# Kernel optimization log

Hardware: AMD Instinct MI355X
Metric: run time of the kernel (lower is better)

## Reference

```python
import jax, jax.numpy as jnp
import numpy as np

N = 300000
MAX_TORSION = 7
MAX_RIGID = 8
MAX_SS = 3
MAX_ATOM = 24
NRES = 22
EPS = 1e-6


def v_norm_safe(v):
    # normalize last dim with epsilon clamp (torch v_norm_safe analogue)
    return v / jnp.clip(jnp.linalg.norm(v, axis=-1, keepdims=True), EPS)


def combine_operations(X, Y):
    # X, Y: [..., 4, 3] rigid ops (3x3 rotation rows + 1 translation row)
    rot = X[..., :3, :] @ Y[..., :3, :]
    t = jnp.einsum('...ij,...j->...i', X[..., :3, :], Y[..., 3, :]) + X[..., 3, :]
    return jnp.concatenate([rot, t[..., None, :]], axis=-2)


def setup_inputs() -> dict:
    key = jax.random.key(0)
    ks = jax.random.split(key, 9)
    return {
        'output_0': jax.random.normal(ks[0], (N, 2 * MAX_TORSION + MAX_SS, 1), jnp.float32),
        'output_1': jax.random.normal(ks[1], (N, 3, 3), jnp.float32),
        'pos': jax.random.normal(ks[2], (N, 3), jnp.float32),
        'ss': jax.random.randint(ks[3], (N,), 0, MAX_SS),
        'residue_type': jax.random.randint(ks[4], (N,), 0, NRES),
        'rigid_transforms': jax.random.normal(ks[5], (MAX_SS, NRES, MAX_RIGID, 4, 3), jnp.float32),
        'rigid_groups': jax.random.normal(ks[6], (MAX_SS, NRES, MAX_ATOM, 3), jnp.float32),
        'transforms_dep': jax.random.randint(ks[7], (NRES, MAX_RIGID), 0, MAX_RIGID),
        'rigids_dep': jax.random.randint(ks[8], (NRES, MAX_ATOM), 0, MAX_RIGID),
    }


def reference(output_0, output_1, pos, ss, residue_type,
              rigid_transforms, rigid_groups, transforms_dep, rigids_dep):
    # ---- StructureModule.output_to_opr_6D ----
    bb0 = output_1[:, :2]                                   # [N,2,3]
    e0 = v_norm_safe(bb0[:, 0])
    v1 = bb0[:, 1]
    u1 = v1 - e0 * jnp.sum(e0 * v1, axis=-1, keepdims=True)
    e1 = v_norm_safe(u1)
    e2 = jnp.cross(e0, e1)
    rot = jnp.stack([e0, e1, e2], axis=1).swapaxes(-1, -2)  # [N,3,3]
    t = 0.1 * output_1[:, 2][:, None, :]                    # [N,1,3]
    bb = jnp.concatenate([rot, t], axis=1)                  # [N,4,3]
    sc = v_norm_safe(output_0[:, :2 * MAX_TORSION].reshape(-1, MAX_TORSION, 2))

    # ---- build_structure ----
    transforms = rigid_transforms[ss, residue_type]         # [N,8,4,3]
    rigids = rigid_groups[ss, residue_type]                 # [N,24,3]
    tdep = transforms_dep[residue_type]                     # [N,8]
    rdep = rigids_dep[residue_type]                         # [N,24]

    n = output_0.shape[0]
    c, s = sc[..., 0], sc[..., 1]                           # [N,7]
    zr = jnp.zeros_like(c)
    on = jnp.ones_like(c)
    tor_rot = jnp.stack([
        jnp.stack([on, zr, zr], axis=-1),
        jnp.stack([zr, c, -s], axis=-1),
        jnp.stack([zr, s, c], axis=-1),
    ], axis=-2)                                             # [N,7,3,3]
    tor = jnp.concatenate(
        [tor_rot, jnp.zeros((n, MAX_TORSION, 1, 3), output_0.dtype)], axis=2)
    opr0 = jnp.concatenate([bb[:, :3], (bb[:, 3] + pos)[:, None]], axis=1)  # [N,4,3]
    opr = jnp.concatenate([opr0[:, None], tor], axis=1)     # [N,8,4,3]

    opr = combine_operations(transforms, opr)
    for i_tor in range(1, MAX_RIGID):                       # fixed 7-step dependency chain
        prev = jnp.take_along_axis(opr, tdep[:, i_tor][:, None, None, None], axis=1)[:, 0]
        opr = opr.at[:, i_tor].set(combine_operations(prev, opr[:, i_tor]))

    opr_g = jnp.take_along_axis(opr, rdep[:, :, None, None], axis=1)  # [N,24,4,3]
    R = jnp.einsum('naij,naj->nai', opr_g[:, :, :3], rigids) + opr_g[:, :, 3]
    return (R, opr[:, 0])
```

## Files before the change

### kernel.cpp

```cpp
#include <hip/hip_runtime.h>
#include <math.h>

#define NRES 22

__device__ __forceinline__ void sel8(const float (&fr)[8][12], int d, float (&P)[12]) {
    const bool b0 = (d & 1) != 0;
    const bool b1 = (d & 2) != 0;
    const bool b2 = (d & 4) != 0;
#pragma unroll
    for (int k = 0; k < 12; ++k) {
        float a01 = b0 ? fr[1][k] : fr[0][k];
        float a23 = b0 ? fr[3][k] : fr[2][k];
        float a45 = b0 ? fr[5][k] : fr[4][k];
        float a67 = b0 ? fr[7][k] : fr[6][k];
        float b03 = b1 ? a23 : a01;
        float b47 = b1 ? a67 : a45;
        P[k] = b2 ? b47 : b03;
    }
}

__device__ __forceinline__ void apply_point(const float (&F)[12], float x, float y, float z,
                                            float &px, float &py, float &pz) {
    px = fmaf(F[0], x, fmaf(F[1], y, fmaf(F[2], z, F[9])));
    py = fmaf(F[3], x, fmaf(F[4], y, fmaf(F[5], z, F[10])));
    pz = fmaf(F[6], x, fmaf(F[7], y, fmaf(F[8], z, F[11])));
}

extern "C" __global__ __launch_bounds__(256)
void model_kernel(const float* __restrict__ o0,
                  const float* __restrict__ o1,
                  const float* __restrict__ pos,
                  const int*   __restrict__ ssArr,
                  const int*   __restrict__ rtArr,
                  const float* __restrict__ rigT,
                  const float* __restrict__ rigG,
                  const int*   __restrict__ tdepArr,
                  const int*   __restrict__ rdepArr,
                  float* __restrict__ outR,
                  float* __restrict__ outF,
                  int N)
{
    const int res = blockIdx.x * 256 + threadIdx.x;
    if (res >= N) return;

    const int s  = ssArr[res];
    const int rt = rtArr[res];

    float c[7], sn[7];
    const float* o0p = o0 + (size_t)res * 17;
#pragma unroll
    for (int t = 0; t < 7; ++t) {
        float cr = o0p[2 * t], sr = o0p[2 * t + 1];
        float n2 = cr * cr + sr * sr;
        float inv = rsqrtf(fmaxf(n2, 1e-12f));
        c[t]  = cr * inv;
        sn[t] = sr * inv;
    }

    const float* o1p = o1 + (size_t)res * 9;
    float r0x = o1p[0], r0y = o1p[1], r0z = o1p[2];
    float v1x = o1p[3], v1y = o1p[4], v1z = o1p[5];
    float t2x = o1p[6], t2y = o1p[7], t2z = o1p[8];
    float inv0 = rsqrtf(fmaxf(r0x * r0x + r0y * r0y + r0z * r0z, 1e-12f));
    float e0x = r0x * inv0, e0y = r0y * inv0, e0z = r0z * inv0;
    float d01 = e0x * v1x + e0y * v1y + e0z * v1z;
    float u1x = v1x - e0x * d01, u1y = v1y - e0y * d01, u1z = v1z - e0z * d01;
    float inv1 = rsqrtf(fmaxf(u1x * u1x + u1y * u1y + u1z * u1z, 1e-12f));
    float e1x = u1x * inv1, e1y = u1y * inv1, e1z = u1z * inv1;
    float e2x = e0y * e1z - e0z * e1y;
    float e2y = e0z * e1x - e0x * e1z;
    float e2z = e0x * e1y - e0y * e1x;
    const float* pp = pos + (size_t)res * 3;
    float btx = 0.1f * t2x + pp[0];
    float bty = 0.1f * t2y + pp[1];
    float btz = 0.1f * t2z + pp[2];

    const int sr22 = s * NRES + rt;
    const float4* T4 = (const float4*)rigT + (size_t)sr22 * 24;

    float fr[8][12];

    {
        float4 q0 = T4[0], q1 = T4[1], q2 = T4[2];
        float T0[12] = {q0.x, q0.y, q0.z, q0.w, q1.x, q1.y, q1.z, q1.w,
                        q2.x, q2.y, q2.z, q2.w};
#pragma unroll
        for (int i = 0; i < 3; ++i) {
            float a = T0[i * 3 + 0], b = T0[i * 3 + 1], d = T0[i * 3 + 2];
            fr[0][i * 3 + 0] = a * e0x + b * e0y + d * e0z;
            fr[0][i * 3 + 1] = a * e1x + b * e1y + d * e1z;
            fr[0][i * 3 + 2] = a * e2x + b * e2y + d * e2z;
            fr[0][9 + i]     = a * btx + b * bty + d * btz + T0[9 + i];
        }
    }

#pragma unroll
    for (int f = 1; f < 8; ++f) {
        float4 q0 = T4[f * 3 + 0], q1 = T4[f * 3 + 1], q2 = T4[f * 3 + 2];
        float Tf[12] = {q0.x, q0.y, q0.z, q0.w, q1.x, q1.y, q1.z, q1.w,
                        q2.x, q2.y, q2.z, q2.w};
        float cc = c[f - 1], ssn = sn[f - 1];
#pragma unroll
        for (int i = 0; i < 3; ++i) {
            fr[f][i * 3 + 0] = Tf[i * 3 + 0];
            fr[f][i * 3 + 1] = Tf[i * 3 + 1] * cc + Tf[i * 3 + 2] * ssn;
            fr[f][i * 3 + 2] = Tf[i * 3 + 2] * cc - Tf[i * 3 + 1] * ssn;
            fr[f][9 + i]     = Tf[9 + i];
        }
    }

    int tdv[8];
    {
        const int4* tdq = (const int4*)(tdepArr + rt * 8);
        int4 a = tdq[0], b = tdq[1];
        tdv[0] = a.x; tdv[1] = a.y; tdv[2] = a.z; tdv[3] = a.w;
        tdv[4] = b.x; tdv[5] = b.y; tdv[6] = b.z; tdv[7] = b.w;
    }
#pragma unroll
    for (int i = 1; i < 8; ++i) {
        float P[12];
        sel8(fr, tdv[i] & 7, P);
        float Y[12];
#pragma unroll
        for (int k = 0; k < 12; ++k) Y[k] = fr[i][k];
#pragma unroll
        for (int r = 0; r < 3; ++r) {
            float a = P[r * 3 + 0], b = P[r * 3 + 1], d = P[r * 3 + 2];
#pragma unroll
            for (int j = 0; j < 3; ++j)
                fr[i][r * 3 + j] = a * Y[j] + b * Y[3 + j] + d * Y[6 + j];
            fr[i][9 + r] = a * Y[9] + b * Y[10] + d * Y[11] + P[9 + r];
        }
    }

    const float4* G4  = (const float4*)rigG + (size_t)sr22 * 18;
    const int4*   RD4 = (const int4*)(rdepArr + rt * 24);
    float4* OR4 = (float4*)(outR + (size_t)res * 72);
#pragma unroll
    for (int ck = 0; ck < 6; ++ck) {
        int4 rd = RD4[ck];
        float4 g0 = G4[ck * 3 + 0], g1 = G4[ck * 3 + 1], g2 = G4[ck * 3 + 2];
        float P[12];
        float p0x, p0y, p0z, p1x, p1y, p1z, p2x, p2y, p2z, p3x, p3y, p3z;
        sel8(fr, rd.x & 7, P); apply_point(P, g0.x, g0.y, g0.z, p0x, p0y, p0z);
        sel8(fr, rd.y & 7, P); apply_point(P, g0.w, g1.x, g1.y, p1x, p1y, p1z);
        sel8(fr, rd.z & 7, P); apply_point(P, g1.z, g1.w, g2.x, p2x, p2y, p2z);
        sel8(fr, rd.w & 7, P); apply_point(P, g2.y, g2.z, g2.w, p3x, p3y, p3z);
        OR4[ck * 3 + 0] = make_float4(p0x, p0y, p0z, p1x);
        OR4[ck * 3 + 1] = make_float4(p1y, p1z, p2x, p2y);
        OR4[ck * 3 + 2] = make_float4(p2z, p3x, p3y, p3z);
    }

    float4* OF4 = (float4*)(outF + (size_t)res * 12);
    OF4[0] = make_float4(fr[0][0], fr[0][1], fr[0][2], fr[0][3]);
    OF4[1] = make_float4(fr[0][4], fr[0][5], fr[0][6], fr[0][7]);
    OF4[2] = make_float4(fr[0][8], fr[0][9], fr[0][10], fr[0][11]);
}

extern "C" void kernel_launch(void* const* d_in, const int* in_sizes, int n_in,
                              void* d_out, int out_size, void* d_ws, size_t ws_size,
                              hipStream_t stream) {
    const float* o0   = (const float*)d_in[0];
    const float* o1   = (const float*)d_in[1];
    const float* pos  = (const float*)d_in[2];
    const int*   ssA  = (const int*)d_in[3];
    const int*   rtA  = (const int*)d_in[4];
    const float* rigT = (const float*)d_in[5];
    const float* rigG = (const float*)d_in[6];
    const int*   tdep = (const int*)d_in[7];
    const int*   rdep = (const int*)d_in[8];

    const int N = in_sizes[3];
    float* outR = (float*)d_out;
    float* outF = (float*)d_out + (size_t)N * 72;

    const int block = 256;
    const int grid  = (N + block - 1) / block;
    model_kernel<<<grid, block, 0, stream>>>(o0, o1, pos, ssA, rtA, rigT, rigG,
                                             tdep, rdep, outR, outF, N);
}
```

Measured before the change: 187.2 us.

## Stage lookup tables and coalesced per-residue inputs through shared memory

Each block now copies the full rigid transform, rigid group and dependency tables into padded LDS, and stages the per-residue o0, o1 and pos rows through LDS with coalesced float4 loads. Threads then read their inputs and table entries from LDS instead of doing strided, data-dependent global gathers. The cost is about 64KB of LDS per block, which limits occupancy, plus roughly 50KB of table reload per block and extra barriers.

```diff
diff --git a/kernel.cpp b/kernel.cpp
--- a/kernel.cpp
+++ b/kernel.cpp
@@ -2,6 +2,13 @@
 #include <math.h>
 
 #define NRES 22
+
+#define L_RIGT 0
+#define L_RIGG 6402
+#define L_TDEP 11220
+#define L_RDEP 11418
+#define L_STRM 11968
+#define L_TOT  16320
 
 __device__ __forceinline__ void sel8(const float (&fr)[8][12], int d, float (&P)[12]) {
     const bool b0 = (d & 1) != 0;
@@ -40,24 +47,85 @@
                   float* __restrict__ outF,
                   int N)
 {
-    const int res = blockIdx.x * 256 + threadIdx.x;
-    if (res >= N) return;
+    __shared__ float lds[L_TOT];
+    int* ilds = (int*)lds;
+
+    const int tid = threadIdx.x;
+    const int R0  = blockIdx.x << 8;
+    const int cnt = min(256, N - R0);
+
+    for (int i = tid; i < 1584; i += 256) {
+        float4 v = ((const float4*)rigT)[i];
+        int g = i << 2;
+        int c = g / 96;
+        int base = L_RIGT + c * 97 + (g - c * 96);
+        lds[base] = v.x; lds[base + 1] = v.y; lds[base + 2] = v.z; lds[base + 3] = v.w;
+    }
+    for (int i = tid; i < 1188; i += 256) {
+        float4 v = ((const float4*)rigG)[i];
+        int g = i << 2;
+        int c = g / 72;
+        int base = L_RIGG + c * 73 + (g - c * 72);
+        lds[base] = v.x; lds[base + 1] = v.y; lds[base + 2] = v.z; lds[base + 3] = v.w;
+    }
+    for (int i = tid; i < 176; i += 256) {
+        int r = i >> 3;
+        ilds[L_TDEP + r * 9 + (i & 7)] = tdepArr[i];
+    }
+    for (int i = tid; i < 528; i += 256) {
+        int r = i / 24;
+        ilds[L_RDEP + r * 25 + (i - r * 24)] = rdepArr[i];
+    }
+    if (cnt == 256) {
+        const float4* src = (const float4*)(o0 + (size_t)R0 * 17);
+        float4* dst = (float4*)(lds + L_STRM);
+        for (int i = tid; i < 1088; i += 256) dst[i] = src[i];
+    } else {
+        for (int i = tid; i < cnt * 17; i += 256) lds[L_STRM + i] = o0[(size_t)R0 * 17 + i];
+    }
+    __syncthreads();
+
+    float c7[7], s7[7];
+    {
+        const float* my = lds + L_STRM + tid * 17;
+        if (tid < cnt) {
+#pragma unroll
+            for (int t = 0; t < 7; ++t) {
+                float cr = my[2 * t], sr = my[2 * t + 1];
+                float inv = rsqrtf(fmaxf(cr * cr + sr * sr, 1e-12f));
+                c7[t] = cr * inv;
+                s7[t] = sr * inv;
+            }
+        }
+    }
+    __syncthreads();
+
+    if (cnt == 256) {
+        const float4* s1 = (const float4*)(o1 + (size_t)R0 * 9);
+        float4* d1 = (float4*)(lds + L_STRM);
+        for (int i = tid; i < 576; i += 256) d1[i] = s1[i];
+        const float4* s2 = (const float4*)(pos + (size_t)R0 * 3);
+        float4* d2 = (float4*)(lds + L_STRM + 2304);
+        for (int i = tid; i < 192; i += 256) d2[i] = s2[i];
+    } else {
+        for (int i = tid; i < cnt * 9; i += 256) lds[L_STRM + i] = o1[(size_t)R0 * 9 + i];
+        for (int i = tid; i < cnt * 3; i += 256) lds[L_STRM + 2304 + i] = pos[(size_t)R0 * 3 + i];
+    }
+    __syncthreads();
+
+    if (tid >= cnt) return;
+    const int res = R0 + tid;
 
     const int s  = ssArr[res];
     const int rt = rtArr[res];
-
-    float c[7], sn[7];
-    const float* o0p = o0 + (size_t)res * 17;
-#pragma unroll
-    for (int t = 0; t < 7; ++t) {
-        float cr = o0p[2 * t], sr = o0p[2 * t + 1];
-        float n2 = cr * cr + sr * sr;
-        float inv = rsqrtf(fmaxf(n2, 1e-12f));
-        c[t]  = cr * inv;
-        sn[t] = sr * inv;
-    }
-
-    const float* o1p = o1 + (size_t)res * 9;
+    const int cmb = s * NRES + rt;
+    const float* Tp = lds + L_RIGT + cmb * 97;
+    const float* Gp = lds + L_RIGG + cmb * 73;
+    const int*   td = ilds + L_TDEP + rt * 9;
+    const int*   rd = ilds + L_RDEP + rt * 25;
+
+    const float* o1p = lds + L_STRM + tid * 9;
+    const float* pp  = lds + L_STRM + 2304 + tid * 3;
     float r0x = o1p[0], r0y = o1p[1], r0z = o1p[2];
     float v1x = o1p[3], v1y = o1p[4], v1z = o1p[5];
     float t2x = o1p[6], t2y = o1p[7], t2z = o1p[8];
@@ -70,56 +138,39 @@
     float e2x = e0y * e1z - e0z * e1y;
     float e2y = e0z * e1x - e0x * e1z;
     float e2z = e0x * e1y - e0y * e1x;
-    const float* pp = pos + (size_t)res * 3;
     float btx = 0.1f * t2x + pp[0];
     float bty = 0.1f * t2y + pp[1];
     float btz = 0.1f * t2z + pp[2];
 
-    const int sr22 = s * NRES + rt;
-    const float4* T4 = (const float4*)rigT + (size_t)sr22 * 24;
-
     float fr[8][12];
 
-    {
-        float4 q0 = T4[0], q1 = T4[1], q2 = T4[2];
-        float T0[12] = {q0.x, q0.y, q0.z, q0.w, q1.x, q1.y, q1.z, q1.w,
-                        q2.x, q2.y, q2.z, q2.w};
+#pragma unroll
+    for (int i = 0; i < 3; ++i) {
+        float a = Tp[i * 3 + 0], b = Tp[i * 3 + 1], d = Tp[i * 3 + 2];
+        fr[0][i * 3 + 0] = a * e0x + b * e0y + d * e0z;
+        fr[0][i * 3 + 1] = a * e1x + b * e1y + d * e1z;
+        fr[0][i * 3 + 2] = a * e2x + b * e2y + d * e2z;
+        fr[0][9 + i]     = a * btx + b * bty + d * btz + Tp[9 + i];
+    }
+
+#pragma unroll
+    for (int f = 1; f < 8; ++f) {
+        const float* Tf = Tp + f * 12;
+        float cc = c7[f - 1], ssn = s7[f - 1];
 #pragma unroll
         for (int i = 0; i < 3; ++i) {
-            float a = T0[i * 3 + 0], b = T0[i * 3 + 1], d = T0[i * 3 + 2];
-            fr[0][i * 3 + 0] = a * e0x + b * e0y + d * e0z;
-            fr[0][i * 3 + 1] = a * e1x + b * e1y + d * e1z;
-            fr[0][i * 3 + 2] = a * e2x + b * e2y + d * e2z;
-            fr[0][9 + i]     = a * btx + b * bty + d * btz + T0[9 + i];
-        }
-    }
-
-#pragma unroll
-    for (int f = 1; f < 8; ++f) {
-        float4 q0 = T4[f * 3 + 0], q1 = T4[f * 3 + 1], q2 = T4[f * 3 + 2];
-        float Tf[12] = {q0.x, q0.y, q0.z, q0.w, q1.x, q1.y, q1.z, q1.w,
-                        q2.x, q2.y, q2.z, q2.w};
-        float cc = c[f - 1], ssn = sn[f - 1];
-#pragma unroll
-        for (int i = 0; i < 3; ++i) {
+            float m1 = Tf[i * 3 + 1], m2 = Tf[i * 3 + 2];
             fr[f][i * 3 + 0] = Tf[i * 3 + 0];
-            fr[f][i * 3 + 1] = Tf[i * 3 + 1] * cc + Tf[i * 3 + 2] * ssn;
-            fr[f][i * 3 + 2] = Tf[i * 3 + 2] * cc - Tf[i * 3 + 1] * ssn;
+            fr[f][i * 3 + 1] = m1 * cc + m2 * ssn;
+            fr[f][i * 3 + 2] = m2 * cc - m1 * ssn;
             fr[f][9 + i]     = Tf[9 + i];
         }
     }
 
-    int tdv[8];
-    {
-        const int4* tdq = (const int4*)(tdepArr + rt * 8);
-        int4 a = tdq[0], b = tdq[1];
-        tdv[0] = a.x; tdv[1] = a.y; tdv[2] = a.z; tdv[3] = a.w;
-        tdv[4] = b.x; tdv[5] = b.y; tdv[6] = b.z; tdv[7] = b.w;
-    }
 #pragma unroll
     for (int i = 1; i < 8; ++i) {
         float P[12];
-        sel8(fr, tdv[i] & 7, P);
+        sel8(fr, td[i] & 7, P);
         float Y[12];
 #pragma unroll
         for (int k = 0; k < 12; ++k) Y[k] = fr[i][k];
@@ -133,19 +184,18 @@
         }
     }
 
-    const float4* G4  = (const float4*)rigG + (size_t)sr22 * 18;
-    const int4*   RD4 = (const int4*)(rdepArr + rt * 24);
     float4* OR4 = (float4*)(outR + (size_t)res * 72);
 #pragma unroll
     for (int ck = 0; ck < 6; ++ck) {
-        int4 rd = RD4[ck];
-        float4 g0 = G4[ck * 3 + 0], g1 = G4[ck * 3 + 1], g2 = G4[ck * 3 + 2];
+        int r0 = rd[ck * 4 + 0] & 7, r1 = rd[ck * 4 + 1] & 7;
+        int r2 = rd[ck * 4 + 2] & 7, r3 = rd[ck * 4 + 3] & 7;
+        const float* g = Gp + ck * 12;
         float P[12];
         float p0x, p0y, p0z, p1x, p1y, p1z, p2x, p2y, p2z, p3x, p3y, p3z;
-        sel8(fr, rd.x & 7, P); apply_point(P, g0.x, g0.y, g0.z, p0x, p0y, p0z);
-        sel8(fr, rd.y & 7, P); apply_point(P, g0.w, g1.x, g1.y, p1x, p1y, p1z);
-        sel8(fr, rd.z & 7, P); apply_point(P, g1.z, g1.w, g2.x, p2x, p2y, p2z);
-        sel8(fr, rd.w & 7, P); apply_point(P, g2.y, g2.z, g2.w, p3x, p3y, p3z);
+        sel8(fr, r0, P); apply_point(P, g[0], g[1], g[2],  p0x, p0y, p0z);
+        sel8(fr, r1, P); apply_point(P, g[3], g[4], g[5],  p1x, p1y, p1z);
+        sel8(fr, r2, P); apply_point(P, g[6], g[7], g[8],  p2x, p2y, p2z);
+        sel8(fr, r3, P); apply_point(P, g[9], g[10], g[11], p3x, p3y, p3z);
         OR4[ck * 3 + 0] = make_float4(p0x, p0y, p0z, p1x);
         OR4[ck * 3 + 1] = make_float4(p1y, p1z, p2x, p2y);
         OR4[ck * 3 + 2] = make_float4(p2z, p3x, p3y, p3z);
```

New measurement: 214.6 us. +14.6%, slower.

## Split into per-residue frame chain kernel and per-atom kernel with bf16 frames

Applied to the files above, without the earlier changes.

Splits the monolithic kernel in two. The first kernel computes the eight frames per residue and stores them as bf16 in workspace. The second runs one thread per atom, using coalesced-ish scalar stores and no dynamic 8-way register select. This is meant to remove the heavy per-thread select cost and the strided 288-byte per-thread output writes, but it adds a workspace round trip, a second launch, and bf16 rounding of the frames, which lowers output precision. The monolithic kernel is kept as a fallback for when the workspace is too small.

```diff
diff --git a/kernel.cpp b/kernel.cpp
--- a/kernel.cpp
+++ b/kernel.cpp
@@ -1,4 +1,5 @@
 #include <hip/hip_runtime.h>
+#include <hip/hip_bf16.h>
 #include <math.h>
 
 #define NRES 22
@@ -26,17 +27,21 @@
     pz = fmaf(F[6], x, fmaf(F[7], y, fmaf(F[8], z, F[11])));
 }
 
+__device__ __forceinline__ unsigned pk2(float a, float b) {
+    __hip_bfloat162 h = __float22bfloat162_rn(make_float2(a, b));
+    union { __hip_bfloat162 h; unsigned u; } cv; cv.h = h;
+    return cv.u;
+}
+
 extern "C" __global__ __launch_bounds__(256)
-void model_kernel(const float* __restrict__ o0,
+void chain_kernel(const float* __restrict__ o0,
                   const float* __restrict__ o1,
                   const float* __restrict__ pos,
                   const int*   __restrict__ ssArr,
                   const int*   __restrict__ rtArr,
                   const float* __restrict__ rigT,
-                  const float* __restrict__ rigG,
                   const int*   __restrict__ tdepArr,
-                  const int*   __restrict__ rdepArr,
-                  float* __restrict__ outR,
+                  unsigned* __restrict__ framesPk,
                   float* __restrict__ outF,
                   int N)
 {
@@ -51,8 +56,7 @@
 #pragma unroll
     for (int t = 0; t < 7; ++t) {
         float cr = o0p[2 * t], sr = o0p[2 * t + 1];
-        float n2 = cr * cr + sr * sr;
-        float inv = rsqrtf(fmaxf(n2, 1e-12f));
+        float inv = rsqrtf(fmaxf(cr * cr + sr * sr, 1e-12f));
         c[t]  = cr * inv;
         sn[t] = sr * inv;
     }
@@ -102,9 +106,10 @@
         float cc = c[f - 1], ssn = sn[f - 1];
 #pragma unroll
         for (int i = 0; i < 3; ++i) {
+            float m1 = Tf[i * 3 + 1], m2 = Tf[i * 3 + 2];
             fr[f][i * 3 + 0] = Tf[i * 3 + 0];
-            fr[f][i * 3 + 1] = Tf[i * 3 + 1] * cc + Tf[i * 3 + 2] * ssn;
-            fr[f][i * 3 + 2] = Tf[i * 3 + 2] * cc - Tf[i * 3 + 1] * ssn;
+            fr[f][i * 3 + 1] = m1 * cc + m2 * ssn;
+            fr[f][i * 3 + 2] = m2 * cc - m1 * ssn;
             fr[f][9 + i]     = Tf[9 + i];
         }
     }
@@ -133,6 +138,156 @@
         }
     }
 
+    float4* OF4 = (float4*)(outF + (size_t)res * 12);
+    OF4[0] = make_float4(fr[0][0], fr[0][1], fr[0][2], fr[0][3]);
+    OF4[1] = make_float4(fr[0][4], fr[0][5], fr[0][6], fr[0][7]);
+    OF4[2] = make_float4(fr[0][8], fr[0][9], fr[0][10], fr[0][11]);
+
+    const float* fl = &fr[0][0];
+    uint4* dst = (uint4*)(framesPk + (size_t)res * 48);
+#pragma unroll
+    for (int j = 0; j < 12; ++j) {
+        uint4 w;
+        w.x = pk2(fl[8 * j + 0], fl[8 * j + 1]);
+        w.y = pk2(fl[8 * j + 2], fl[8 * j + 3]);
+        w.z = pk2(fl[8 * j + 4], fl[8 * j + 5]);
+        w.w = pk2(fl[8 * j + 6], fl[8 * j + 7]);
+        dst[j] = w;
+    }
+}
+
+extern "C" __global__ __launch_bounds__(256)
+void atoms_kernel(const int*   __restrict__ ssArr,
+                  const int*   __restrict__ rtArr,
+                  const float* __restrict__ rigG,
+                  const int*   __restrict__ rdepArr,
+                  const unsigned* __restrict__ framesPk,
+                  float* __restrict__ outR,
+                  int N)
+{
+    const int gid = blockIdx.x * 256 + threadIdx.x;
+    if (gid >= N * 24) return;
+    const unsigned t8 = (unsigned)gid >> 3;
+    const unsigned res = (unsigned)(((unsigned long long)t8 * 0xAAAAAAABull) >> 33);
+    const int a = gid - (int)res * 24;
+
+    const int s  = ssArr[res];
+    const int rt = rtArr[res];
+    const int cmb = s * NRES + rt;
+    const int f = rdepArr[rt * 24 + a] & 7;
+
+    const uint2* fp = (const uint2*)(framesPk + (size_t)res * 48 + f * 6);
+    uint2 u0 = fp[0], u1 = fp[1], u2 = fp[2];
+    float F[12];
+    F[0]  = __uint_as_float(u0.x << 16);  F[1]  = __uint_as_float(u0.x & 0xFFFF0000u);
+    F[2]  = __uint_as_float(u0.y << 16);  F[3]  = __uint_as_float(u0.y & 0xFFFF0000u);
+    F[4]  = __uint_as_float(u1.x << 16);  F[5]  = __uint_as_float(u1.x & 0xFFFF0000u);
+    F[6]  = __uint_as_float(u1.y << 16);  F[7]  = __uint_as_float(u1.y & 0xFFFF0000u);
+    F[8]  = __uint_as_float(u2.x << 16);  F[9]  = __uint_as_float(u2.x & 0xFFFF0000u);
+    F[10] = __uint_as_float(u2.y << 16);  F[11] = __uint_as_float(u2.y & 0xFFFF0000u);
+
+    const float* g = rigG + (size_t)cmb * 72 + a * 3;
+    float gx = g[0], gy = g[1], gz = g[2];
+
+    float px = fmaf(F[0], gx, fmaf(F[1], gy, fmaf(F[2], gz, F[9])));
+    float py = fmaf(F[3], gx, fmaf(F[4], gy, fmaf(F[5], gz, F[10])));
+    float pz = fmaf(F[6], gx, fmaf(F[7], gy, fmaf(F[8], gz, F[11])));
+
+    float* o = outR + (size_t)gid * 3;
+    o[0] = px; o[1] = py; o[2] = pz;
+}
+
+extern "C" __global__ __launch_bounds__(256)
+void model_kernel_mono(const float* __restrict__ o0, const float* __restrict__ o1,
+                       const float* __restrict__ pos, const int* __restrict__ ssArr,
+                       const int* __restrict__ rtArr, const float* __restrict__ rigT,
+                       const float* __restrict__ rigG, const int* __restrict__ tdepArr,
+                       const int* __restrict__ rdepArr, float* __restrict__ outR,
+                       float* __restrict__ outF, int N)
+{
+    const int res = blockIdx.x * 256 + threadIdx.x;
+    if (res >= N) return;
+    const int s  = ssArr[res];
+    const int rt = rtArr[res];
+    float c[7], sn[7];
+    const float* o0p = o0 + (size_t)res * 17;
+#pragma unroll
+    for (int t = 0; t < 7; ++t) {
+        float cr = o0p[2 * t], sr = o0p[2 * t + 1];
+        float inv = rsqrtf(fmaxf(cr * cr + sr * sr, 1e-12f));
+        c[t] = cr * inv; sn[t] = sr * inv;
+    }
+    const float* o1p = o1 + (size_t)res * 9;
+    float r0x = o1p[0], r0y = o1p[1], r0z = o1p[2];
+    float v1x = o1p[3], v1y = o1p[4], v1z = o1p[5];
+    float t2x = o1p[6], t2y = o1p[7], t2z = o1p[8];
+    float inv0 = rsqrtf(fmaxf(r0x * r0x + r0y * r0y + r0z * r0z, 1e-12f));
+    float e0x = r0x * inv0, e0y = r0y * inv0, e0z = r0z * inv0;
+    float d01 = e0x * v1x + e0y * v1y + e0z * v1z;
+    float u1x = v1x - e0x * d01, u1y = v1y - e0y * d01, u1z = v1z - e0z * d01;
+    float inv1 = rsqrtf(fmaxf(u1x * u1x + u1y * u1y + u1z * u1z, 1e-12f));
+    float e1x = u1x * inv1, e1y = u1y * inv1, e1z = u1z * inv1;
+    float e2x = e0y * e1z - e0z * e1y;
+    float e2y = e0z * e1x - e0x * e1z;
+    float e2z = e0x * e1y - e0y * e1x;
+    const float* pp = pos + (size_t)res * 3;
+    float btx = 0.1f * t2x + pp[0];
+    float bty = 0.1f * t2y + pp[1];
+    float btz = 0.1f * t2z + pp[2];
+    const int sr22 = s * NRES + rt;
+    const float4* T4 = (const float4*)rigT + (size_t)sr22 * 24;
+    float fr[8][12];
+    {
+        float4 q0 = T4[0], q1 = T4[1], q2 = T4[2];
+        float T0[12] = {q0.x, q0.y, q0.z, q0.w, q1.x, q1.y, q1.z, q1.w,
+                        q2.x, q2.y, q2.z, q2.w};
+#pragma unroll
+        for (int i = 0; i < 3; ++i) {
+            float a = T0[i * 3 + 0], b = T0[i * 3 + 1], d = T0[i * 3 + 2];
+            fr[0][i * 3 + 0] = a * e0x + b * e0y + d * e0z;
+            fr[0][i * 3 + 1] = a * e1x + b * e1y + d * e1z;
+            fr[0][i * 3 + 2] = a * e2x + b * e2y + d * e2z;
+            fr[0][9 + i]     = a * btx + b * bty + d * btz + T0[9 + i];
+        }
+    }
+#pragma unroll
+    for (int f = 1; f < 8; ++f) {
+        float4 q0 = T4[f * 3 + 0], q1 = T4[f * 3 + 1], q2 = T4[f * 3 + 2];
+        float Tf[12] = {q0.x, q0.y, q0.z, q0.w, q1.x, q1.y, q1.z, q1.w,
+                        q2.x, q2.y, q2.z, q2.w};
+        float cc = c[f - 1], ssn = sn[f - 1];
+#pragma unroll
+        for (int i = 0; i < 3; ++i) {
+            float m1 = Tf[i * 3 + 1], m2 = Tf[i * 3 + 2];
+            fr[f][i * 3 + 0] = Tf[i * 3 + 0];
+            fr[f][i * 3 + 1] = m1 * cc + m2 * ssn;
+            fr[f][i * 3 + 2] = m2 * cc - m1 * ssn;
+            fr[f][9 + i]     = Tf[9 + i];
+        }
+    }
+    int tdv[8];
+    {
+        const int4* tdq = (const int4*)(tdepArr + rt * 8);
+        int4 a = tdq[0], b = tdq[1];
+        tdv[0] = a.x; tdv[1] = a.y; tdv[2] = a.z; tdv[3] = a.w;
+        tdv[4] = b.x; tdv[5] = b.y; tdv[6] = b.z; tdv[7] = b.w;
+    }
+#pragma unroll
+    for (int i = 1; i < 8; ++i) {
+        float P[12];
+        sel8(fr, tdv[i] & 7, P);
+        float Y[12];
+#pragma unroll
+        for (int k = 0; k < 12; ++k) Y[k] = fr[i][k];
+#pragma unroll
+        for (int r = 0; r < 3; ++r) {
+            float a = P[r * 3 + 0], b = P[r * 3 + 1], d = P[r * 3 + 2];
+#pragma unroll
+            for (int j = 0; j < 3; ++j)
+                fr[i][r * 3 + j] = a * Y[j] + b * Y[3 + j] + d * Y[6 + j];
+            fr[i][9 + r] = a * Y[9] + b * Y[10] + d * Y[11] + P[9 + r];
+        }
+    }
     const float4* G4  = (const float4*)rigG + (size_t)sr22 * 18;
     const int4*   RD4 = (const int4*)(rdepArr + rt * 24);
     float4* OR4 = (float4*)(outR + (size_t)res * 72);
@@ -150,7 +305,6 @@
         OR4[ck * 3 + 1] = make_float4(p1y, p1z, p2x, p2y);
         OR4[ck * 3 + 2] = make_float4(p2z, p3x, p3y, p3z);
     }
-
     float4* OF4 = (float4*)(outF + (size_t)res * 12);
     OF4[0] = make_float4(fr[0][0], fr[0][1], fr[0][2], fr[0][3]);
     OF4[1] = make_float4(fr[0][4], fr[0][5], fr[0][6], fr[0][7]);
@@ -174,8 +328,22 @@
     float* outR = (float*)d_out;
     float* outF = (float*)d_out + (size_t)N * 72;
 
-    const int block = 256;
-    const int grid  = (N + block - 1) / block;
-    model_kernel<<<grid, block, 0, stream>>>(o0, o1, pos, ssA, rtA, rigT, rigG,
-                                             tdep, rdep, outR, outF, N);
-}
+    const size_t wsNeed = (size_t)N * 192;
+    if (ws_size >= wsNeed) {
+        unsigned* framesPk = (unsigned*)d_ws;
+        const int blockA = 256;
+        const int gridA  = (N + blockA - 1) / blockA;
+        chain_kernel<<<gridA, blockA, 0, stream>>>(o0, o1, pos, ssA, rtA, rigT,
+                                                   tdep, framesPk, outF, N);
+        const int blockB = 256;
+        const long long na = (long long)N * 24;
+        const int gridB  = (int)((na + blockB - 1) / blockB);
+        atoms_kernel<<<gridB, blockB, 0, stream>>>(ssA, rtA, rigG, rdep,
+                                                   framesPk, outR, N);
+    } else {
+        const int block = 256;
+        const int grid  = (N + block - 1) / block;
+        model_kernel_mono<<<grid, block, 0, stream>>>(o0, o1, pos, ssA, rtA, rigT,
+                                                      rigG, tdep, rdep, outR, outF, N);
+    }
+}
```

New measurement: 196.5 us. 1.05x slower.

## Stage per-residue inputs and frames through LDS for coalesced loads and stores

Applied to the files above, without the earlier changes.

Each 256-thread block now handles 64 residues. The block cooperatively loads the o0/o1/pos rows into shared memory with coalesced float4 reads. One thread per residue builds the 8 frames and writes them to LDS, then all 256 threads split the 24 atoms per residue and write outputs with consecutive addresses. This removes the strided per-thread global loads and stores of the old one-thread-per-residue layout. In exchange, only a quarter of the threads are active during the frame chain, and the kernel adds two barriers and LDS bank traffic.

```diff
diff --git a/kernel.cpp b/kernel.cpp
--- a/kernel.cpp
+++ b/kernel.cpp
@@ -2,6 +2,14 @@
 #include <math.h>
 
 #define NRES 22
+#define RPB  64
+
+#define L_FR   0
+#define L_O0   6272
+#define L_O1   7360
+#define L_POS  7936
+#define L_META 8128
+#define L_TOT  8192
 
 __device__ __forceinline__ void sel8(const float (&fr)[8][12], int d, float (&P)[12]) {
     const bool b0 = (d & 1) != 0;
@@ -17,13 +25,6 @@
         float b47 = b1 ? a67 : a45;
         P[k] = b2 ? b47 : b03;
     }
-}
-
-__device__ __forceinline__ void apply_point(const float (&F)[12], float x, float y, float z,
-                                            float &px, float &py, float &pz) {
-    px = fmaf(F[0], x, fmaf(F[1], y, fmaf(F[2], z, F[9])));
-    py = fmaf(F[3], x, fmaf(F[4], y, fmaf(F[5], z, F[10])));
-    pz = fmaf(F[6], x, fmaf(F[7], y, fmaf(F[8], z, F[11])));
 }
 
 extern "C" __global__ __launch_bounds__(256)
@@ -40,121 +41,177 @@
                   float* __restrict__ outF,
                   int N)
 {
-    const int res = blockIdx.x * 256 + threadIdx.x;
-    if (res >= N) return;
-
-    const int s  = ssArr[res];
-    const int rt = rtArr[res];
-
-    float c[7], sn[7];
-    const float* o0p = o0 + (size_t)res * 17;
-#pragma unroll
-    for (int t = 0; t < 7; ++t) {
-        float cr = o0p[2 * t], sr = o0p[2 * t + 1];
-        float n2 = cr * cr + sr * sr;
-        float inv = rsqrtf(fmaxf(n2, 1e-12f));
-        c[t]  = cr * inv;
-        sn[t] = sr * inv;
-    }
-
-    const float* o1p = o1 + (size_t)res * 9;
-    float r0x = o1p[0], r0y = o1p[1], r0z = o1p[2];
-    float v1x = o1p[3], v1y = o1p[4], v1z = o1p[5];
-    float t2x = o1p[6], t2y = o1p[7], t2z = o1p[8];
-    float inv0 = rsqrtf(fmaxf(r0x * r0x + r0y * r0y + r0z * r0z, 1e-12f));
-    float e0x = r0x * inv0, e0y = r0y * inv0, e0z = r0z * inv0;
-    float d01 = e0x * v1x + e0y * v1y + e0z * v1z;
-    float u1x = v1x - e0x * d01, u1y = v1y - e0y * d01, u1z = v1z - e0z * d01;
-    float inv1 = rsqrtf(fmaxf(u1x * u1x + u1y * u1y + u1z * u1z, 1e-12f));
-    float e1x = u1x * inv1, e1y = u1y * inv1, e1z = u1z * inv1;
-    float e2x = e0y * e1z - e0z * e1y;
-    float e2y = e0z * e1x - e0x * e1z;
-    float e2z = e0x * e1y - e0y * e1x;
-    const float* pp = pos + (size_t)res * 3;
-    float btx = 0.1f * t2x + pp[0];
-    float bty = 0.1f * t2y + pp[1];
-    float btz = 0.1f * t2z + pp[2];
-
-    const int sr22 = s * NRES + rt;
-    const float4* T4 = (const float4*)rigT + (size_t)sr22 * 24;
-
-    float fr[8][12];
-
-    {
-        float4 q0 = T4[0], q1 = T4[1], q2 = T4[2];
-        float T0[12] = {q0.x, q0.y, q0.z, q0.w, q1.x, q1.y, q1.z, q1.w,
-                        q2.x, q2.y, q2.z, q2.w};
-#pragma unroll
-        for (int i = 0; i < 3; ++i) {
-            float a = T0[i * 3 + 0], b = T0[i * 3 + 1], d = T0[i * 3 + 2];
-            fr[0][i * 3 + 0] = a * e0x + b * e0y + d * e0z;
-            fr[0][i * 3 + 1] = a * e1x + b * e1y + d * e1z;
-            fr[0][i * 3 + 2] = a * e2x + b * e2y + d * e2z;
-            fr[0][9 + i]     = a * btx + b * bty + d * btz + T0[9 + i];
-        }
-    }
-
-#pragma unroll
-    for (int f = 1; f < 8; ++f) {
-        float4 q0 = T4[f * 3 + 0], q1 = T4[f * 3 + 1], q2 = T4[f * 3 + 2];
-        float Tf[12] = {q0.x, q0.y, q0.z, q0.w, q1.x, q1.y, q1.z, q1.w,
-                        q2.x, q2.y, q2.z, q2.w};
-        float cc = c[f - 1], ssn = sn[f - 1];
-#pragma unroll
-        for (int i = 0; i < 3; ++i) {
-            fr[f][i * 3 + 0] = Tf[i * 3 + 0];
-            fr[f][i * 3 + 1] = Tf[i * 3 + 1] * cc + Tf[i * 3 + 2] * ssn;
-            fr[f][i * 3 + 2] = Tf[i * 3 + 2] * cc - Tf[i * 3 + 1] * ssn;
-            fr[f][9 + i]     = Tf[9 + i];
-        }
-    }
-
-    int tdv[8];
-    {
-        const int4* tdq = (const int4*)(tdepArr + rt * 8);
-        int4 a = tdq[0], b = tdq[1];
-        tdv[0] = a.x; tdv[1] = a.y; tdv[2] = a.z; tdv[3] = a.w;
-        tdv[4] = b.x; tdv[5] = b.y; tdv[6] = b.z; tdv[7] = b.w;
-    }
-#pragma unroll
-    for (int i = 1; i < 8; ++i) {
-        float P[12];
-        sel8(fr, tdv[i] & 7, P);
-        float Y[12];
-#pragma unroll
-        for (int k = 0; k < 12; ++k) Y[k] = fr[i][k];
-#pragma unroll
-        for (int r = 0; r < 3; ++r) {
-            float a = P[r * 3 + 0], b = P[r * 3 + 1], d = P[r * 3 + 2];
-#pragma unroll
-            for (int j = 0; j < 3; ++j)
-                fr[i][r * 3 + j] = a * Y[j] + b * Y[3 + j] + d * Y[6 + j];
-            fr[i][9 + r] = a * Y[9] + b * Y[10] + d * Y[11] + P[9 + r];
-        }
-    }
-
-    const float4* G4  = (const float4*)rigG + (size_t)sr22 * 18;
-    const int4*   RD4 = (const int4*)(rdepArr + rt * 24);
-    float4* OR4 = (float4*)(outR + (size_t)res * 72);
-#pragma unroll
-    for (int ck = 0; ck < 6; ++ck) {
-        int4 rd = RD4[ck];
-        float4 g0 = G4[ck * 3 + 0], g1 = G4[ck * 3 + 1], g2 = G4[ck * 3 + 2];
-        float P[12];
-        float p0x, p0y, p0z, p1x, p1y, p1z, p2x, p2y, p2z, p3x, p3y, p3z;
-        sel8(fr, rd.x & 7, P); apply_point(P, g0.x, g0.y, g0.z, p0x, p0y, p0z);
-        sel8(fr, rd.y & 7, P); apply_point(P, g0.w, g1.x, g1.y, p1x, p1y, p1z);
-        sel8(fr, rd.z & 7, P); apply_point(P, g1.z, g1.w, g2.x, p2x, p2y, p2z);
-        sel8(fr, rd.w & 7, P); apply_point(P, g2.y, g2.z, g2.w, p3x, p3y, p3z);
-        OR4[ck * 3 + 0] = make_float4(p0x, p0y, p0z, p1x);
-        OR4[ck * 3 + 1] = make_float4(p1y, p1z, p2x, p2y);
-        OR4[ck * 3 + 2] = make_float4(p2z, p3x, p3y, p3z);
-    }
-
-    float4* OF4 = (float4*)(outF + (size_t)res * 12);
-    OF4[0] = make_float4(fr[0][0], fr[0][1], fr[0][2], fr[0][3]);
-    OF4[1] = make_float4(fr[0][4], fr[0][5], fr[0][6], fr[0][7]);
-    OF4[2] = make_float4(fr[0][8], fr[0][9], fr[0][10], fr[0][11]);
+    __shared__ float lds[L_TOT];
+    int* ilds = (int*)lds;
+
+    const int tid = threadIdx.x;
+    const int R0  = blockIdx.x * RPB;
+    const int cnt = min(RPB, N - R0);
+
+    if (cnt == RPB) {
+        const float4* s0v = (const float4*)(o0 + (size_t)R0 * 17);
+        float4* d0v = (float4*)(lds + L_O0);
+        d0v[tid & 255] = s0v[tid & 255];
+        if (tid < 16) d0v[256 + tid] = s0v[256 + tid];
+        if (tid < 144) {
+            ((float4*)(lds + L_O1))[tid] = ((const float4*)(o1 + (size_t)R0 * 9))[tid];
+        }
+        if (tid < 48) {
+            ((float4*)(lds + L_POS))[tid] = ((const float4*)(pos + (size_t)R0 * 3))[tid];
+        }
+    } else {
+        for (int i = tid; i < cnt * 17; i += 256) lds[L_O0 + i]  = o0[(size_t)R0 * 17 + i];
+        for (int i = tid; i < cnt * 9;  i += 256) lds[L_O1 + i]  = o1[(size_t)R0 * 9 + i];
+        for (int i = tid; i < cnt * 3;  i += 256) lds[L_POS + i] = pos[(size_t)R0 * 3 + i];
+    }
+    if (tid < cnt) {
+        int s = ssArr[R0 + tid];
+        int r = rtArr[R0 + tid];
+        ilds[L_META + tid] = (s * NRES + r) | (r << 16);
+    }
+    __syncthreads();
+
+    if (tid < RPB && tid < cnt) {
+        const int l = tid;
+        const int meta = ilds[L_META + l];
+        const int cmb  = meta & 0xFFFF;
+        const int rtv  = meta >> 16;
+
+        float c[7], sn[7];
+        const float* myo0 = lds + L_O0 + l * 17;
+#pragma unroll
+        for (int t = 0; t < 7; ++t) {
+            float cr = myo0[2 * t], sr = myo0[2 * t + 1];
+            float inv = rsqrtf(fmaxf(cr * cr + sr * sr, 1e-12f));
+            c[t]  = cr * inv;
+            sn[t] = sr * inv;
+        }
+
+        const float* o1p = lds + L_O1 + l * 9;
+        const float* pp  = lds + L_POS + l * 3;
+        float r0x = o1p[0], r0y = o1p[1], r0z = o1p[2];
+        float v1x = o1p[3], v1y = o1p[4], v1z = o1p[5];
+        float t2x = o1p[6], t2y = o1p[7], t2z = o1p[8];
+        float inv0 = rsqrtf(fmaxf(r0x * r0x + r0y * r0y + r0z * r0z, 1e-12f));
+        float e0x = r0x * inv0, e0y = r0y * inv0, e0z = r0z * inv0;
+        float d01 = e0x * v1x + e0y * v1y + e0z * v1z;
+        float u1x = v1x - e0x * d01, u1y = v1y - e0y * d01, u1z = v1z - e0z * d01;
+        float inv1 = rsqrtf(fmaxf(u1x * u1x + u1y * u1y + u1z * u1z, 1e-12f));
+        float e1x = u1x * inv1, e1y = u1y * inv1, e1z = u1z * inv1;
+        float e2x = e0y * e1z - e0z * e1y;
+        float e2y = e0z * e1x - e0x * e1z;
+        float e2z = e0x * e1y - e0y * e1x;
+        float btx = 0.1f * t2x + pp[0];
+        float bty = 0.1f * t2y + pp[1];
+        float btz = 0.1f * t2z + pp[2];
+
+        const float4* T4 = (const float4*)rigT + (size_t)cmb * 24;
+        float fr[8][12];
+
+        {
+            float4 q0 = T4[0], q1 = T4[1], q2 = T4[2];
+            float T0[12] = {q0.x, q0.y, q0.z, q0.w, q1.x, q1.y, q1.z, q1.w,
+                            q2.x, q2.y, q2.z, q2.w};
+#pragma unroll
+            for (int i = 0; i < 3; ++i) {
+                float a = T0[i * 3 + 0], b = T0[i * 3 + 1], d = T0[i * 3 + 2];
+                fr[0][i * 3 + 0] = a * e0x + b * e0y + d * e0z;
+                fr[0][i * 3 + 1] = a * e1x + b * e1y + d * e1z;
+                fr[0][i * 3 + 2] = a * e2x + b * e2y + d * e2z;
+                fr[0][9 + i]     = a * btx + b * bty + d * btz + T0[9 + i];
+            }
+        }
+#pragma unroll
+        for (int f = 1; f < 8; ++f) {
+            float4 q0 = T4[f * 3 + 0], q1 = T4[f * 3 + 1], q2 = T4[f * 3 + 2];
+            float Tf[12] = {q0.x, q0.y, q0.z, q0.w, q1.x, q1.y, q1.z, q1.w,
+                            q2.x, q2.y, q2.z, q2.w};
+            float cc = c[f - 1], ssn = sn[f - 1];
+#pragma unroll
+            for (int i = 0; i < 3; ++i) {
+                float m1 = Tf[i * 3 + 1], m2 = Tf[i * 3 + 2];
+                fr[f][i * 3 + 0] = Tf[i * 3 + 0];
+                fr[f][i * 3 + 1] = m1 * cc + m2 * ssn;
+                fr[f][i * 3 + 2] = m2 * cc - m1 * ssn;
+                fr[f][9 + i]     = Tf[9 + i];
+            }
+        }
+
+        int tdv[8];
+        {
+            const int4* tdq = (const int4*)(tdepArr + rtv * 8);
+            int4 a = tdq[0], b = tdq[1];
+            tdv[0] = a.x; tdv[1] = a.y; tdv[2] = a.z; tdv[3] = a.w;
+            tdv[4] = b.x; tdv[5] = b.y; tdv[6] = b.z; tdv[7] = b.w;
+        }
+#pragma unroll
+        for (int i = 1; i < 8; ++i) {
+            float P[12];
+            sel8(fr, tdv[i] & 7, P);
+            float Y[12];
+#pragma unroll
+            for (int k = 0; k < 12; ++k) Y[k] = fr[i][k];
+#pragma unroll
+            for (int r = 0; r < 3; ++r) {
+                float a = P[r * 3 + 0], b = P[r * 3 + 1], d = P[r * 3 + 2];
+#pragma unroll
+                for (int j = 0; j < 3; ++j)
+                    fr[i][r * 3 + j] = a * Y[j] + b * Y[3 + j] + d * Y[6 + j];
+                fr[i][9 + r] = a * Y[9] + b * Y[10] + d * Y[11] + P[9 + r];
+            }
+        }
+
+        float* fb = lds + L_FR + l * 98;
+#pragma unroll
+        for (int f = 0; f < 8; ++f) {
+#pragma unroll
+            for (int j = 0; j < 6; ++j) {
+                *(float2*)(fb + f * 12 + 2 * j) =
+                    make_float2(fr[f][2 * j], fr[f][2 * j + 1]);
+            }
+        }
+    }
+    __syncthreads();
+
+#pragma unroll
+    for (int k2 = 0; k2 < 3; ++k2) {
+        int t2 = tid + 256 * k2;
+        if (t2 < cnt * 12) {
+            int q = t2 / 12;
+            int k = t2 - q * 12;
+            outF[(size_t)R0 * 12 + t2] = lds[L_FR + q * 98 + k];
+        }
+    }
+
+#pragma unroll
+    for (int kk = 0; kk < 6; ++kk) {
+        int ag = tid + 256 * kk;
+        if (ag < cnt * 24) {
+            int q = ag / 24;
+            int a = ag - q * 24;
+            int meta = ilds[L_META + q];
+            int cmb  = meta & 0xFFFF;
+            int rtv  = meta >> 16;
+            int f = rdepArr[rtv * 24 + a] & 7;
+
+            const float* fb = lds + L_FR + q * 98 + f * 12;
+            float F[12];
+#pragma unroll
+            for (int j = 0; j < 6; ++j) {
+                float2 v = *(const float2*)(fb + 2 * j);
+                F[2 * j] = v.x; F[2 * j + 1] = v.y;
+            }
+            const float* g = rigG + (size_t)cmb * 72 + a * 3;
+            float gx = g[0], gy = g[1], gz = g[2];
+
+            float px = fmaf(F[0], gx, fmaf(F[1], gy, fmaf(F[2], gz, F[9])));
+            float py = fmaf(F[3], gx, fmaf(F[4], gy, fmaf(F[5], gz, F[10])));
+            float pz = fmaf(F[6], gx, fmaf(F[7], gy, fmaf(F[8], gz, F[11])));
+
+            float* o = outR + (size_t)R0 * 72 + (size_t)ag * 3;
+            o[0] = px; o[1] = py; o[2] = pz;
+        }
+    }
 }
 
 extern "C" void kernel_launch(void* const* d_in, const int* in_sizes, int n_in,
@@ -174,8 +231,7 @@
     float* outR = (float*)d_out;
     float* outF = (float*)d_out + (size_t)N * 72;
 
-    const int block = 256;
-    const int grid  = (N + block - 1) / block;
-    model_kernel<<<grid, block, 0, stream>>>(o0, o1, pos, ssA, rtA, rigT, rigG,
-                                             tdep, rdep, outR, outF, N);
+    const int grid = (N + RPB - 1) / RPB;
+    model_kernel<<<grid, 256, 0, stream>>>(o0, o1, pos, ssA, rtA, rigT, rigG,
+                                           tdep, rdep, outR, outF, N);
 }
```

New measurement: 201.1 us. +7.4%, slower.
